# Optimization experiments

Measured on AMD Instinct MI355X. Metric: run time of the kernel, lower is better.

Reference implementation:

```python
import jax, jax.numpy as jnp
import numpy as np

NEG_INF = -1e30  # stand-in for -inf that is safe under fp16/bf16 softmax


def setup_inputs() -> dict:
    key = jax.random.key(0)
    k1, k2, k3, k4, k5 = jax.random.split(key, 5)
    B, Tq, Tk, DIN, DOUT = 8, 1024, 4096, 1024, 256
    dec = jax.random.normal(k1, (B, Tq, DIN), dtype=jnp.float32)
    emb = jax.random.normal(k2, (B, Tk, DOUT), dtype=jnp.float32)
    emask = jax.random.randint(k3, (B, Tk), 0, 2, dtype=jnp.int32)
    W = jax.random.normal(k4, (DOUT, DIN), dtype=jnp.float32) * (1.0 / np.sqrt(DIN))
    b = jax.random.normal(k5, (DOUT,), dtype=jnp.float32) * 0.01
    return {"dec": dec, "emb": emb, "emask": emask, "W": W, "b": b}


def reference(dec, emb, emask, W, b):
    # Linear projection: [B,Tq,DIN] @ [DIN,DOUT] + b -> [B,Tq,DOUT]
    decsmall = jnp.einsum('bqi,oi->bqo', dec, W) + b
    # Scores: [B,Tq,Tk]
    unnorm = jnp.einsum('bqo,bko->bqk', decsmall, emb)
    # mask: positions where emask == 0 are disallowed
    masked = jnp.where((emask == 0)[:, None, :], NEG_INF, unnorm)
    attn = jax.nn.softmax(masked, axis=2)
    out = jnp.einsum('bqk,bko->bqo', attn, emb)
    return (out, attn)
```

## Files before the change

### kernel.cpp

```cpp
#include <hip/hip_runtime.h>
#include <hip/hip_bf16.h>
#include <hip/hip_fp16.h>

typedef unsigned short u16;
typedef __attribute__((ext_vector_type(8))) short short8;
typedef __attribute__((ext_vector_type(8))) u16 u16x8;
typedef __attribute__((ext_vector_type(4))) u16 u16x4;
typedef __attribute__((ext_vector_type(8))) _Float16 half8;
typedef __attribute__((ext_vector_type(4))) float f32x4;

#define NB 8
#define TQn 1024
#define TKn 4096
#define DINn 1024
#define DOUTn 256
#define NROWS (NB * TQn)
#define NKB (TKn / 128)
#define EXPSHIFT 40.0f
#define LP 40

#define DEV static __device__ __forceinline__

DEV u16 f2bf(float x) {
    __hip_bfloat16 h = __float2bfloat16(x);
    return *reinterpret_cast<u16*>(&h);
}
DEV float bf2f(u16 u) {
    __hip_bfloat16 h;
    *reinterpret_cast<u16*>(&h) = u;
    return __bfloat162float(h);
}
DEV void split2(float x, u16& hi, u16& lo) {
    u16 h = f2bf(x);
    float hf = bf2f(h);
    hi = h;
    lo = f2bf(x - hf);
}
DEV void split4(const float4 v, u16x4& h, u16x4& l) {
    u16 h0, l0, h1, l1, h2, l2, h3, l3;
    split2(v.x, h0, l0);
    split2(v.y, h1, l1);
    split2(v.z, h2, l2);
    split2(v.w, h3, l3);
    h = (u16x4){h0, h1, h2, h3};
    l = (u16x4){l0, l1, l2, l3};
}
DEV short8 ld8s(const u16* p) { return *reinterpret_cast<const short8*>(p); }
DEV half8 ld8h(const u16* p) { return *reinterpret_cast<const half8*>(p); }
DEV void st8(u16* p, u16x8 v) { *reinterpret_cast<u16x8*>(p) = v; }

__global__ __launch_bounds__(256) void k_embT(const float* __restrict__ emb,
                                              _Float16* __restrict__ embT) {
    __shared__ float tile[64][65];
    const int b = blockIdx.z;
    const int k0 = blockIdx.x * 64;
    const int o0 = blockIdx.y * 64;
    const int t = threadIdx.x;
    const int c = t & 63;
    const int r0 = t >> 6;
#pragma unroll
    for (int i = 0; i < 16; i++) {
        int r = r0 + i * 4;
        tile[c][r] = emb[((size_t)b * TKn + k0 + r) * DOUTn + o0 + c];
    }
    __syncthreads();
#pragma unroll
    for (int i = 0; i < 16; i++) {
        int r = r0 + i * 4;
        embT[((size_t)b * DOUTn + o0 + r) * TKn + k0 + c] = (_Float16)tile[r][c];
    }
}

__global__ __launch_bounds__(256) void k_linear(const float* __restrict__ dec,
                                                const float* __restrict__ W,
                                                const float* __restrict__ bias,
                                                u16* __restrict__ ds_hi,
                                                u16* __restrict__ ds_lo) {
    __shared__ u16 sAh[128][LP], sAl[128][LP], sBh[64][LP], sBl[64][LP];
    const int t = threadIdx.x;
    const int m0 = blockIdx.x * 128;
    const int n0 = blockIdx.y * 64;
    const int w = t >> 6, lane = t & 63;
    const int wr = w >> 1, wc = w & 1;
    const int lr = lane & 15, g = lane >> 4, kg8 = g * 8;

    f32x4 acc[4][2];
#pragma unroll
    for (int m = 0; m < 4; m++)
#pragma unroll
        for (int n = 0; n < 2; n++) acc[m][n] = (f32x4){0.f, 0.f, 0.f, 0.f};

    for (int k0 = 0; k0 < DINn; k0 += 32) {
        __syncthreads();
#pragma unroll
        for (int i = 0; i < 4; i++) {
            int f = i * 256 + t;
            int row = f >> 3, c4 = (f & 7) * 4;
            const float4 v = *reinterpret_cast<const float4*>(
                dec + (size_t)(m0 + row) * DINn + k0 + c4);
            u16x4 h, l;
            split4(v, h, l);
            *reinterpret_cast<u16x4*>(&sAh[row][c4]) = h;
            *reinterpret_cast<u16x4*>(&sAl[row][c4]) = l;
        }
#pragma unroll
        for (int i = 0; i < 2; i++) {
            int f = i * 256 + t;
            int row = f >> 3, c4 = (f & 7) * 4;
            const float4 v = *reinterpret_cast<const float4*>(
                W + (size_t)(n0 + row) * DINn + k0 + c4);
            u16x4 h, l;
            split4(v, h, l);
            *reinterpret_cast<u16x4*>(&sBh[row][c4]) = h;
            *reinterpret_cast<u16x4*>(&sBl[row][c4]) = l;
        }
        __syncthreads();
        short8 ah[4], al[4], bh[2], bl[2];
#pragma unroll
        for (int m = 0; m < 4; m++) {
            int row = wr * 64 + m * 16 + lr;
            ah[m] = ld8s(&sAh[row][kg8]);
            al[m] = ld8s(&sAl[row][kg8]);
        }
#pragma unroll
        for (int n = 0; n < 2; n++) {
            int row = wc * 32 + n * 16 + lr;
            bh[n] = ld8s(&sBh[row][kg8]);
            bl[n] = ld8s(&sBl[row][kg8]);
        }
#pragma unroll
        for (int m = 0; m < 4; m++)
#pragma unroll
            for (int n = 0; n < 2; n++) {
                acc[m][n] = __builtin_amdgcn_mfma_f32_16x16x32_bf16(ah[m], bh[n], acc[m][n], 0, 0, 0);
                acc[m][n] = __builtin_amdgcn_mfma_f32_16x16x32_bf16(ah[m], bl[n], acc[m][n], 0, 0, 0);
                acc[m][n] = __builtin_amdgcn_mfma_f32_16x16x32_bf16(al[m], bh[n], acc[m][n], 0, 0, 0);
            }
    }
#pragma unroll
    for (int m = 0; m < 4; m++) {
#pragma unroll
        for (int n = 0; n < 2; n++) {
            int colg = n0 + wc * 32 + n * 16 + lr;
            float bv = bias[colg];
#pragma unroll
            for (int r = 0; r < 4; r++) {
                int rowg = m0 + wr * 64 + m * 16 + g * 4 + r;
                float v = acc[m][n][r] + bv;
                u16 h, l;
                split2(v, h, l);
                ds_hi[(size_t)rowg * DOUTn + colg] = h;
                ds_lo[(size_t)rowg * DOUTn + colg] = l;
            }
        }
    }
}

__global__ __launch_bounds__(256) void k_scores_exp(const u16* __restrict__ ds_hi,
                                                    const u16* __restrict__ ds_lo,
                                                    const float* __restrict__ emb,
                                                    const int* __restrict__ emask,
                                                    float* __restrict__ attn,
                                                    float* __restrict__ partsum) {
    __shared__ u16 sAh[128][LP], sAl[128][LP], sBh[128][LP], sBl[128][LP];
    __shared__ float sSum[2][128];
    const int t = threadIdx.x;
    const int flat = blockIdx.x + 8 * (blockIdx.y + 32 * blockIdx.z);
    const int b = flat & 7;
    const int rest = flat >> 3;
    const int kb = rest & 31;
    const int q0 = (rest >> 5) * 128;
    const int kb0 = kb * 128;
    const int w = t >> 6, lane = t & 63;
    const int wr = w >> 1, wc = w & 1;
    const int lr = lane & 15, g = lane >> 4, kg8 = g * 8;

    f32x4 acc[4][4];
#pragma unroll
    for (int m = 0; m < 4; m++)
#pragma unroll
        for (int n = 0; n < 4; n++) acc[m][n] = (f32x4){0.f, 0.f, 0.f, 0.f};

    for (int o0 = 0; o0 < DOUTn; o0 += 32) {
        __syncthreads();
#pragma unroll
        for (int i = 0; i < 2; i++) {
            int f8 = i * 256 + t;
            int row = f8 >> 2, c8 = (f8 & 3) * 8;
            size_t src = (size_t)(b * TQn + q0 + row) * DOUTn + o0 + c8;
            st8(&sAh[row][c8], *reinterpret_cast<const u16x8*>(ds_hi + src));
            st8(&sAl[row][c8], *reinterpret_cast<const u16x8*>(ds_lo + src));
        }
#pragma unroll
        for (int i = 0; i < 4; i++) {
            int f = i * 256 + t;
            int row = f >> 3, c4 = (f & 7) * 4;
            const float4 v = *reinterpret_cast<const float4*>(
                emb + (size_t)(b * TKn + kb0 + row) * DOUTn + o0 + c4);
            u16x4 h, l;
            split4(v, h, l);
            *reinterpret_cast<u16x4*>(&sBh[row][c4]) = h;
            *reinterpret_cast<u16x4*>(&sBl[row][c4]) = l;
        }
        __syncthreads();
        short8 ah[4], al[4], bh[4], bl[4];
#pragma unroll
        for (int m = 0; m < 4; m++) {
            int row = wr * 64 + m * 16 + lr;
            ah[m] = ld8s(&sAh[row][kg8]);
            al[m] = ld8s(&sAl[row][kg8]);
        }
#pragma unroll
        for (int n = 0; n < 4; n++) {
            int row = wc * 64 + n * 16 + lr;
            bh[n] = ld8s(&sBh[row][kg8]);
            bl[n] = ld8s(&sBl[row][kg8]);
        }
#pragma unroll
        for (int m = 0; m < 4; m++)
#pragma unroll
            for (int n = 0; n < 4; n++) {
                acc[m][n] = __builtin_amdgcn_mfma_f32_16x16x32_bf16(ah[m], bh[n], acc[m][n], 0, 0, 0);
                acc[m][n] = __builtin_amdgcn_mfma_f32_16x16x32_bf16(ah[m], bl[n], acc[m][n], 0, 0, 0);
                acc[m][n] = __builtin_amdgcn_mfma_f32_16x16x32_bf16(al[m], bh[n], acc[m][n], 0, 0, 0);
            }
    }
    const int* em = emask + (size_t)b * TKn;
    float* pout = attn + ((size_t)(b * TQn + q0)) * TKn + kb0;
    float rowAcc[4][4];
#pragma unroll
    for (int m = 0; m < 4; m++)
#pragma unroll
        for (int r = 0; r < 4; r++) rowAcc[m][r] = 0.f;

#pragma unroll
    for (int n = 0; n < 4; n++) {
        int colL = wc * 64 + n * 16 + lr;
        int mk = em[kb0 + colL];
#pragma unroll
        for (int m = 0; m < 4; m++) {
#pragma unroll
            for (int r = 0; r < 4; r++) {
                int rowL = wr * 64 + m * 16 + g * 4 + r;
                float p = mk ? __expf(acc[m][n][r] - EXPSHIFT) : 0.f;
                __builtin_nontemporal_store(p, &pout[(size_t)rowL * TKn + colL]);
                rowAcc[m][r] += p;
            }
        }
    }
#pragma unroll
    for (int m = 0; m < 4; m++) {
#pragma unroll
        for (int r = 0; r < 4; r++) {
            float v = rowAcc[m][r];
            v += __shfl_xor(v, 1);
            v += __shfl_xor(v, 2);
            v += __shfl_xor(v, 4);
            v += __shfl_xor(v, 8);
            if (lr == 0) sSum[wc][wr * 64 + m * 16 + g * 4 + r] = v;
        }
    }
    __syncthreads();
    if (t < 128) {
        partsum[(size_t)kb * NROWS + (size_t)b * TQn + q0 + t] =
            sSum[0][t] + sSum[1][t];
    }
}

__global__ __launch_bounds__(256) void k_rowsum(const float* __restrict__ partsum,
                                                float* __restrict__ inv_sum) {
    int row = blockIdx.x * 256 + threadIdx.x;
    float s = 0.f;
#pragma unroll
    for (int kb = 0; kb < NKB; kb++) s += partsum[(size_t)kb * NROWS + row];
    inv_sum[row] = 1.0f / s;
}

__global__ __launch_bounds__(256) void k_pv7(float* __restrict__ attn,
                                             const _Float16* __restrict__ embT,
                                             const float* __restrict__ inv_sum,
                                             float* __restrict__ partial) {
    __shared__ u16 sA[2][64][LP];
    __shared__ u16 sB[2][256][LP];
    __shared__ float sInv[64];
    const int t = threadIdx.x;
    const int flat = blockIdx.x;
    const int b = flat & 7;
    const int rest = flat >> 3;
    const int kc = rest & 3;
    const int q0 = (rest >> 2) * 64;
    const int w = t >> 6, lane = t & 63;
    const int lr = lane & 15, g = lane >> 4, kg8 = g * 8;
    const int kbase = kc * 1024;
    const size_t rowBase = (size_t)b * TQn + q0;
    const u16* ebt = reinterpret_cast<const u16*>(embT);

    if (t < 64) sInv[t] = inv_sum[rowBase + t];

    const int ar0 = t >> 3, ac4 = (t & 7) * 4;

    f32x4 acc[4][4];
#pragma unroll
    for (int m = 0; m < 4; m++)
#pragma unroll
        for (int n = 0; n < 4; n++) acc[m][n] = (f32x4){0.f, 0.f, 0.f, 0.f};

    f32x4 pa[2];
    u16x8 pb[4];
#pragma unroll
    for (int i = 0; i < 2; i++) {
        int row = ar0 + i * 32;
        pa[i] = *reinterpret_cast<const f32x4*>(attn + (rowBase + row) * TKn + kbase + ac4);
    }
#pragma unroll
    for (int i = 0; i < 4; i++) {
        int f = i * 256 + t;
        int row = f >> 2, c8 = (f & 3) * 8;
        pb[i] = *reinterpret_cast<const u16x8*>(
            ebt + (size_t)(b * DOUTn + row) * TKn + kbase + c8);
    }
    __syncthreads();

    const int NIT = 1024 / 32;
    for (int it = 0; it < NIT; it++) {
        const int cur = it & 1;
        const int ks = it * 32;
#pragma unroll
        for (int i = 0; i < 2; i++) {
            int row = ar0 + i * 32;
            f32x4 v = pa[i] * sInv[row];
            *reinterpret_cast<f32x4*>(attn + (rowBase + row) * TKn + kbase + ks + ac4) = v;
            u16x4 hv;
            hv[0] = __builtin_bit_cast(u16, (_Float16)v[0]);
            hv[1] = __builtin_bit_cast(u16, (_Float16)v[1]);
            hv[2] = __builtin_bit_cast(u16, (_Float16)v[2]);
            hv[3] = __builtin_bit_cast(u16, (_Float16)v[3]);
            *reinterpret_cast<u16x4*>(&sA[cur][row][ac4]) = hv;
        }
#pragma unroll
        for (int i = 0; i < 4; i++) {
            int f = i * 256 + t;
            int row = f >> 2, c8 = (f & 3) * 8;
            st8(&sB[cur][row][c8], pb[i]);
        }
        asm volatile("s_waitcnt lgkmcnt(0)" ::: "memory");
        __builtin_amdgcn_s_barrier();
        asm volatile("" ::: "memory");
        if (it + 1 < NIT) {
            int ksn = ks + 32;
#pragma unroll
            for (int i = 0; i < 2; i++) {
                int row = ar0 + i * 32;
                pa[i] = *reinterpret_cast<const f32x4*>(
                    attn + (rowBase + row) * TKn + kbase + ksn + ac4);
            }
#pragma unroll
            for (int i = 0; i < 4; i++) {
                int f = i * 256 + t;
                int row = f >> 2, c8 = (f & 3) * 8;
                pb[i] = *reinterpret_cast<const u16x8*>(
                    ebt + (size_t)(b * DOUTn + row) * TKn + kbase + ksn + c8);
            }
        }
        half8 a[4], bb[4];
#pragma unroll
        for (int m = 0; m < 4; m++) a[m] = ld8h(&sA[cur][m * 16 + lr][kg8]);
#pragma unroll
        for (int n = 0; n < 4; n++) bb[n] = ld8h(&sB[cur][w * 64 + n * 16 + lr][kg8]);
#pragma unroll
        for (int m = 0; m < 4; m++)
#pragma unroll
            for (int n = 0; n < 4; n++)
                acc[m][n] = __builtin_amdgcn_mfma_f32_16x16x32_f16(a[m], bb[n], acc[m][n], 0, 0, 0);
    }
#pragma unroll
    for (int m = 0; m < 4; m++) {
#pragma unroll
        for (int n = 0; n < 4; n++) {
            int col = w * 64 + n * 16 + lr;
#pragma unroll
            for (int r = 0; r < 4; r++) {
                size_t grow = rowBase + m * 16 + g * 4 + r;
                partial[((size_t)kc * NROWS + grow) * DOUTn + col] = acc[m][n][r];
            }
        }
    }
}

__global__ __launch_bounds__(256) void k_reduce(const float* __restrict__ partial,
                                                float* __restrict__ out) {
    const size_t stride = (size_t)NROWS * DOUTn;
    size_t i = ((size_t)blockIdx.x * 256 + threadIdx.x) * 4;
    f32x4 a0 = *reinterpret_cast<const f32x4*>(partial + i);
    f32x4 a1 = *reinterpret_cast<const f32x4*>(partial + stride + i);
    f32x4 a2 = *reinterpret_cast<const f32x4*>(partial + 2 * stride + i);
    f32x4 a3 = *reinterpret_cast<const f32x4*>(partial + 3 * stride + i);
    f32x4 s = (a0 + a1) + (a2 + a3);
    *reinterpret_cast<f32x4*>(out + i) = s;
}

extern "C" void kernel_launch(void* const* d_in, const int* in_sizes, int n_in,
                              void* d_out, int out_size, void* d_ws, size_t ws_size,
                              hipStream_t stream) {
    const float* dec = (const float*)d_in[0];
    const float* emb = (const float*)d_in[1];
    const int* emask = (const int*)d_in[2];
    const float* W = (const float*)d_in[3];
    const float* bias = (const float*)d_in[4];

    float* out = (float*)d_out;
    float* attn = out + (size_t)NROWS * DOUTn;

    char* wsb = (char*)d_ws;
    u16* ds_hi = (u16*)wsb;
    wsb += (size_t)NROWS * DOUTn * 2;
    u16* ds_lo = (u16*)wsb;
    wsb += (size_t)NROWS * DOUTn * 2;
    _Float16* embT = (_Float16*)wsb;
    wsb += (size_t)NB * DOUTn * TKn * 2;
    float* inv_sum = (float*)wsb;
    wsb += (size_t)NROWS * 4;
    float* partsum = (float*)wsb;
    wsb += (size_t)NKB * NROWS * 4;
    float* partial = (float*)wsb;

    k_embT<<<dim3(TKn / 64, DOUTn / 64, NB), 256, 0, stream>>>(emb, embT);
    k_linear<<<dim3(NROWS / 128, DOUTn / 64), 256, 0, stream>>>(dec, W, bias, ds_hi, ds_lo);
    k_scores_exp<<<dim3(TQn / 128, NKB, NB), 256, 0, stream>>>(ds_hi, ds_lo, emb, emask, attn, partsum);
    k_rowsum<<<dim3(NROWS / 256), 256, 0, stream>>>(partsum, inv_sum);
    k_pv7<<<dim3(512), 256, 0, stream>>>(attn, embT, inv_sum, partial);
    k_reduce<<<dim3((NROWS * DOUTn / 4) / 256), 256, 0, stream>>>(partial, out);
}
```

Before: 229.4 us.

## Enlarge PV tile to 128 rows with 8 waves and split Tk into 8 chunks

The PV kernel now uses 512-thread blocks that each compute a 128x256 output tile, arranged as a 2x4 grid of waves, instead of a 64x256 tile. Tk is split into 8 chunks rather than 4, which keeps the grid at 512 blocks. Each embT tile loaded into shared memory is now reused across twice as many attention rows, halving embT traffic per row. The cost is twice as many fp32 partial outputs to write and then sum in the reduce kernel, which now adds 8 partials instead of 4, and larger shared memory per block that may limit occupancy.

```diff
diff --git a/kernel.cpp b/kernel.cpp
--- a/kernel.cpp
+++ b/kernel.cpp
@@ -16,6 +16,8 @@
 #define DOUTn 256
 #define NROWS (NB * TQn)
 #define NKB (TKn / 128)
+#define NKC 8
+#define KCH (TKn / NKC)
 #define EXPSHIFT 40.0f
 #define LP 40
 
@@ -276,28 +278,29 @@
     inv_sum[row] = 1.0f / s;
 }
 
-__global__ __launch_bounds__(256) void k_pv7(float* __restrict__ attn,
-                                             const _Float16* __restrict__ embT,
-                                             const float* __restrict__ inv_sum,
-                                             float* __restrict__ partial) {
-    __shared__ u16 sA[2][64][LP];
+__global__ __launch_bounds__(512, 4) void k_pv8(float* __restrict__ attn,
+                                                const _Float16* __restrict__ embT,
+                                                const float* __restrict__ inv_sum,
+                                                float* __restrict__ partial) {
+    __shared__ u16 sA[2][128][LP];
     __shared__ u16 sB[2][256][LP];
-    __shared__ float sInv[64];
+    __shared__ float sInv[128];
     const int t = threadIdx.x;
     const int flat = blockIdx.x;
     const int b = flat & 7;
     const int rest = flat >> 3;
-    const int kc = rest & 3;
-    const int q0 = (rest >> 2) * 64;
+    const int kc = rest & 7;
+    const int q0 = (rest >> 3) * 128;
     const int w = t >> 6, lane = t & 63;
     const int lr = lane & 15, g = lane >> 4, kg8 = g * 8;
-    const int kbase = kc * 1024;
+    const int wr = w >> 2, wc = w & 3;
+    const int kbase = kc * KCH;
     const size_t rowBase = (size_t)b * TQn + q0;
     const u16* ebt = reinterpret_cast<const u16*>(embT);
 
-    if (t < 64) sInv[t] = inv_sum[rowBase + t];
-
-    const int ar0 = t >> 3, ac4 = (t & 7) * 4;
+    if (t < 128) sInv[t] = inv_sum[rowBase + t];
+
+    const int ar = t >> 3, ac4 = (t & 7) * 4;
 
     f32x4 acc[4][4];
 #pragma unroll
@@ -306,28 +309,28 @@
         for (int n = 0; n < 4; n++) acc[m][n] = (f32x4){0.f, 0.f, 0.f, 0.f};
 
     f32x4 pa[2];
-    u16x8 pb[4];
+    u16x8 pb[2];
 #pragma unroll
     for (int i = 0; i < 2; i++) {
-        int row = ar0 + i * 32;
+        int row = ar + i * 64;
         pa[i] = *reinterpret_cast<const f32x4*>(attn + (rowBase + row) * TKn + kbase + ac4);
     }
 #pragma unroll
-    for (int i = 0; i < 4; i++) {
-        int f = i * 256 + t;
+    for (int i = 0; i < 2; i++) {
+        int f = i * 512 + t;
         int row = f >> 2, c8 = (f & 3) * 8;
         pb[i] = *reinterpret_cast<const u16x8*>(
             ebt + (size_t)(b * DOUTn + row) * TKn + kbase + c8);
     }
     __syncthreads();
 
-    const int NIT = 1024 / 32;
+    const int NIT = KCH / 32;
     for (int it = 0; it < NIT; it++) {
         const int cur = it & 1;
         const int ks = it * 32;
 #pragma unroll
         for (int i = 0; i < 2; i++) {
-            int row = ar0 + i * 32;
+            int row = ar + i * 64;
             f32x4 v = pa[i] * sInv[row];
             *reinterpret_cast<f32x4*>(attn + (rowBase + row) * TKn + kbase + ks + ac4) = v;
             u16x4 hv;
@@ -338,8 +341,8 @@
             *reinterpret_cast<u16x4*>(&sA[cur][row][ac4]) = hv;
         }
 #pragma unroll
-        for (int i = 0; i < 4; i++) {
-            int f = i * 256 + t;
+        for (int i = 0; i < 2; i++) {
+            int f = i * 512 + t;
             int row = f >> 2, c8 = (f & 3) * 8;
             st8(&sB[cur][row][c8], pb[i]);
         }
@@ -350,13 +353,13 @@
             int ksn = ks + 32;
 #pragma unroll
             for (int i = 0; i < 2; i++) {
-                int row = ar0 + i * 32;
+                int row = ar + i * 64;
                 pa[i] = *reinterpret_cast<const f32x4*>(
                     attn + (rowBase + row) * TKn + kbase + ksn + ac4);
             }
 #pragma unroll
-            for (int i = 0; i < 4; i++) {
-                int f = i * 256 + t;
+            for (int i = 0; i < 2; i++) {
+                int f = i * 512 + t;
                 int row = f >> 2, c8 = (f & 3) * 8;
                 pb[i] = *reinterpret_cast<const u16x8*>(
                     ebt + (size_t)(b * DOUTn + row) * TKn + kbase + ksn + c8);
@@ -364,9 +367,9 @@
         }
         half8 a[4], bb[4];
 #pragma unroll
-        for (int m = 0; m < 4; m++) a[m] = ld8h(&sA[cur][m * 16 + lr][kg8]);
-#pragma unroll
-        for (int n = 0; n < 4; n++) bb[n] = ld8h(&sB[cur][w * 64 + n * 16 + lr][kg8]);
+        for (int m = 0; m < 4; m++) a[m] = ld8h(&sA[cur][wr * 64 + m * 16 + lr][kg8]);
+#pragma unroll
+        for (int n = 0; n < 4; n++) bb[n] = ld8h(&sB[cur][wc * 64 + n * 16 + lr][kg8]);
 #pragma unroll
         for (int m = 0; m < 4; m++)
 #pragma unroll
@@ -377,10 +380,10 @@
     for (int m = 0; m < 4; m++) {
 #pragma unroll
         for (int n = 0; n < 4; n++) {
-            int col = w * 64 + n * 16 + lr;
+            int col = wc * 64 + n * 16 + lr;
 #pragma unroll
             for (int r = 0; r < 4; r++) {
-                size_t grow = rowBase + m * 16 + g * 4 + r;
+                size_t grow = rowBase + wr * 64 + m * 16 + g * 4 + r;
                 partial[((size_t)kc * NROWS + grow) * DOUTn + col] = acc[m][n][r];
             }
         }
@@ -391,11 +394,10 @@
                                                 float* __restrict__ out) {
     const size_t stride = (size_t)NROWS * DOUTn;
     size_t i = ((size_t)blockIdx.x * 256 + threadIdx.x) * 4;
-    f32x4 a0 = *reinterpret_cast<const f32x4*>(partial + i);
-    f32x4 a1 = *reinterpret_cast<const f32x4*>(partial + stride + i);
-    f32x4 a2 = *reinterpret_cast<const f32x4*>(partial + 2 * stride + i);
-    f32x4 a3 = *reinterpret_cast<const f32x4*>(partial + 3 * stride + i);
-    f32x4 s = (a0 + a1) + (a2 + a3);
+    f32x4 s = (f32x4){0.f, 0.f, 0.f, 0.f};
+#pragma unroll
+    for (int kc = 0; kc < NKC; kc++)
+        s += *reinterpret_cast<const f32x4*>(partial + kc * stride + i);
     *reinterpret_cast<f32x4*>(out + i) = s;
 }
 
@@ -428,6 +430,6 @@
     k_linear<<<dim3(NROWS / 128, DOUTn / 64), 256, 0, stream>>>(dec, W, bias, ds_hi, ds_lo);
     k_scores_exp<<<dim3(TQn / 128, NKB, NB), 256, 0, stream>>>(ds_hi, ds_lo, emb, emask, attn, partsum);
     k_rowsum<<<dim3(NROWS / 256), 256, 0, stream>>>(partsum, inv_sum);
-    k_pv7<<<dim3(512), 256, 0, stream>>>(attn, embT, inv_sum, partial);
+    k_pv8<<<dim3(512), 512, 0, stream>>>(attn, embT, inv_sum, partial);
     k_reduce<<<dim3((NROWS * DOUTn / 4) / 256), 256, 0, stream>>>(partial, out);
 }
```

Result: faster. 217.1 us (-5.3%).
